# Kernel optimization log

Hardware: AMD Instinct MI355X
Metric: run time of the kernel (lower is better)

The kernel has to match this reference:

```python
import jax, jax.numpy as jnp
import numpy as np

N_HEADS = 8


def setup_inputs() -> dict:
    key = jax.random.key(0)
    k1, k2 = jax.random.split(key)
    image_qkv = jax.random.normal(k1, (2, 1536, 4096), dtype=jnp.float32)
    st_qkv = jax.random.normal(k2, (2, 1536, 1024), dtype=jnp.float32)
    return {"image_qkv": image_qkv, "st_qkv": st_qkv}


def reference(image_qkv, st_qkv):
    bs, width, img_len = image_qkv.shape
    st_len = st_qkv.shape[2]
    assert width % (3 * N_HEADS) == 0
    ch = width // (3 * N_HEADS)
    hc = N_HEADS * ch

    img_q, img_k, img_v = (image_qkv[:, i * hc:(i + 1) * hc] for i in range(3))
    st_q, st_k, st_v = (st_qkv[:, i * hc:(i + 1) * hc] for i in range(3))

    scale = 1.0 / jnp.sqrt(jnp.sqrt(jnp.float32(ch)))

    def split_heads(x, length):  # [bs, H*ch, L] -> [bs*H, ch, L]
        return x.reshape(bs * N_HEADS, ch, length)

    # image queries attend over st keys/values (softmax applied)
    w_i = jnp.einsum('bct,bcs->bts', split_heads(img_q, img_len) * scale,
                     split_heads(st_k, st_len) * scale)
    w_i = jax.nn.softmax(w_i.astype(jnp.float32), axis=-1).astype(w_i.dtype)
    attn_i = jnp.einsum('bts,bcs->bct', w_i, split_heads(st_v, st_len)).reshape(bs, -1, img_len)

    # st queries attend over image keys/values (NOTE: original code has NO softmax here)
    w_st = jnp.einsum('bct,bcs->bts', split_heads(st_q, st_len) * scale,
                      split_heads(img_k, img_len) * scale)
    attn_st = jnp.einsum('bts,bcs->bct', w_st, split_heads(img_v, img_len)).reshape(bs, -1, st_len)

    return attn_i, attn_st
```

## Files before the change

kernel.cpp:

```cpp
#include <hip/hip_runtime.h>
#include <hip/hip_bf16.h>
#include <stdint.h>

#define DEVI __device__ __forceinline__

typedef __attribute__((ext_vector_type(8))) short short8;
typedef __attribute__((ext_vector_type(16))) float f32x16;
typedef __attribute__((ext_vector_type(4))) float f32x4;
typedef __attribute__((ext_vector_type(2))) unsigned int uint2v;
typedef unsigned short ushortT;

union U8 { short8 s8; unsigned u[4]; };

DEVI unsigned short f2bf(float f) {
  unsigned u = __builtin_bit_cast(unsigned, f);
  u += 0x7fffu + ((u >> 16) & 1u);
  return (unsigned short)(u >> 16);
}
DEVI unsigned pk2(float lo, float hi) {
  return (unsigned)f2bf(lo) | ((unsigned)f2bf(hi) << 16);
}
DEVI unsigned cvtpk(float lo, float hi) {
  unsigned r;
  asm("v_cvt_pk_bf16_f32 %0, %1, %2" : "=v"(r) : "v"(lo), "v"(hi));
  return r;
}
DEVI float exp2a(float x) { return __builtin_amdgcn_exp2f(x); }

#define MFMA32 __builtin_amdgcn_mfma_f32_32x32x16_bf16
#define C_L2E 0.18033688011112042f

__global__ __launch_bounds__(256) void aux_kernel(
    const float* __restrict__ img, const float* __restrict__ st,
    ushortT* __restrict__ kfp, ushortT* __restrict__ vfp,
    float* __restrict__ Mws) {
  __shared__ __align__(16) char pool[32768];
  const int tid = threadIdx.x;
  const int bid = blockIdx.x;
  const int w = tid >> 6, lane = tid & 63, hi = lane >> 5, ln = lane & 31;

  if (bid < 256) {
    const int bh = bid >> 4, t = bid & 15;
    const int b = bh >> 3, h = bh & 7;
    const float* kbase = st + ((size_t)(b * 1536 + 512 + h * 64)) * 1024;
    const float* vbase = st + ((size_t)(b * 1536 + 1024 + h * 64)) * 1024;
    ushortT* ko = kfp + ((size_t)bh * 16 + t) * 4096;
    ushortT* vo = vfp + ((size_t)bh * 16 + t) * 4096;

    float (*kf)[65] = (float (*)[65])pool;
    {
      const int c = tid >> 2, s16 = (tid & 3) * 16;
      const float* kp = kbase + (size_t)c * 1024 + t * 64 + s16;
      f32x4 a = *(const f32x4*)kp, b4 = *(const f32x4*)(kp + 4),
            c4 = *(const f32x4*)(kp + 8), d4 = *(const f32x4*)(kp + 12);
#pragma unroll
      for (int j = 0; j < 4; ++j) {
        kf[c][s16 + j] = a[j];
        kf[c][s16 + 4 + j] = b4[j];
        kf[c][s16 + 8 + j] = c4[j];
        kf[c][s16 + 12 + j] = d4[j];
      }
    }
#pragma unroll
    for (int rep = 0; rep < 2; ++rep) {
      const int pair = tid + rep * 256;
      const int c = pair >> 3, oct = pair & 7;
      const float* vp = vbase + (size_t)c * 1024 + t * 64 + oct * 8;
      f32x4 lo = *(const f32x4*)vp, hp = *(const f32x4*)(vp + 4);
      uint2v la, ha;
      la[0] = pk2(lo[0], lo[1]); la[1] = pk2(lo[2], lo[3]);
      ha[0] = pk2(hp[0], hp[1]); ha[1] = pk2(hp[2], hp[3]);
      const int ci = c >> 5, lnn = c & 31;
      const int ss = oct >> 2, kk2 = (oct >> 1) & 1, o1 = oct & 1;
      const int f = ss * 4 + kk2 * 2 + ci;
      *(uint2v*)(vo + ((size_t)f * 64 + lnn) * 8 + o1 * 4) = la;
      *(uint2v*)(vo + ((size_t)f * 64 + 32 + lnn) * 8 + o1 * 4) = ha;
    }
    __syncthreads();
    {
      const int kk = w;
#pragma unroll
      for (int half = 0; half < 2; ++half) {
        float v8[8];
#pragma unroll
        for (int j = 0; j < 8; ++j) v8[j] = kf[kk * 16 + hi * 8 + j][half * 32 + ln];
        U8 u;
#pragma unroll
        for (int i = 0; i < 4; ++i) u.u[i] = pk2(v8[2 * i], v8[2 * i + 1]);
        *(short8*)(ko + ((size_t)(half * 4 + kk) * 64 + lane) * 8) = u.s8;
      }
    }
  } else {
    const int gb = bid - 256;
    const int bh = gb >> 3, chunk = gb & 7;
    const int b = bh >> 3, h = bh & 7;
    const float* kbase = img + ((size_t)(b * 1536 + 512 + h * 64)) * 4096;
    const float* vbase = img + ((size_t)(b * 1536 + 1024 + h * 64)) * 4096;

    f32x16 m00 = {}, m01 = {}, m10 = {}, m11 = {};
    const int sbeg = chunk * 512 + w * 128;
    for (int s0 = sbeg; s0 < sbeg + 128; s0 += 16) {
      const int sa = s0 + hi * 8;
      short8 av[2], bk[2];
#pragma unroll
      for (int ci = 0; ci < 2; ++ci) {
        const float* vp = vbase + (size_t)(ci * 32 + ln) * 4096 + sa;
        f32x4 lo = *(const f32x4*)vp, hp = *(const f32x4*)(vp + 4);
        U8 u;
        u.u[0] = pk2(lo[0], lo[1]); u.u[1] = pk2(lo[2], lo[3]);
        u.u[2] = pk2(hp[0], hp[1]); u.u[3] = pk2(hp[2], hp[3]);
        av[ci] = u.s8;
      }
#pragma unroll
      for (int cj = 0; cj < 2; ++cj) {
        const float* kp = kbase + (size_t)(cj * 32 + ln) * 4096 + sa;
        f32x4 lo = *(const f32x4*)kp, hp = *(const f32x4*)(kp + 4);
        U8 u;
        u.u[0] = pk2(lo[0], lo[1]); u.u[1] = pk2(lo[2], lo[3]);
        u.u[2] = pk2(hp[0], hp[1]); u.u[3] = pk2(hp[2], hp[3]);
        bk[cj] = u.s8;
      }
      m00 = MFMA32(av[0], bk[0], m00, 0, 0, 0);
      m01 = MFMA32(av[0], bk[1], m01, 0, 0, 0);
      m10 = MFMA32(av[1], bk[0], m10, 0, 0, 0);
      m11 = MFMA32(av[1], bk[1], m11, 0, 0, 0);
    }

    float (*part)[64][64] = (float (*)[64][64])pool;
    if (w < 2) {
#pragma unroll
      for (int q = 0; q < 16; ++q) {
        const int cr = (q & 3) + 8 * (q >> 2) + 4 * hi;
        part[w][cr][ln] = m00[q];
        part[w][cr][32 + ln] = m01[q];
        part[w][32 + cr][ln] = m10[q];
        part[w][32 + cr][32 + ln] = m11[q];
      }
    }
    __syncthreads();
    if (w >= 2) {
      const int pw = w - 2;
#pragma unroll
      for (int q = 0; q < 16; ++q) {
        const int cr = (q & 3) + 8 * (q >> 2) + 4 * hi;
        part[pw][cr][ln] += m00[q];
        part[pw][cr][32 + ln] += m01[q];
        part[pw][32 + cr][ln] += m10[q];
        part[pw][32 + cr][32 + ln] += m11[q];
      }
    }
    __syncthreads();
#pragma unroll
    for (int i = 0; i < 16; ++i) {
      const int e = tid + i * 256;
      const int c = e >> 6, cp = e & 63;
      Mws[(size_t)gb * 4096 + c * 64 + cp] =
          (part[0][c][cp] + part[1][c][cp]) * 0.125f;
    }
  }
}

DEVI void stage_tile(ushortT (*lds)[16][512], int buf, const ushortT* kf_all,
                     const ushortT* vf_all, int fpbase, int lane, int tile) {
#pragma unroll
  for (int j = 0; j < 4; ++j) {
    const int fp = fpbase + j;
    const ushortT* src =
        (fp < 8 ? kf_all + (size_t)tile * 4096 + (size_t)fp * 512
                : vf_all + (size_t)tile * 4096 + (size_t)(fp - 8) * 512) +
        lane * 8;
    __builtin_amdgcn_global_load_lds(
        (const __attribute__((address_space(1))) void*)src,
        (__attribute__((address_space(3))) void*)&lds[buf][fp][0], 16, 0, 0);
  }
}

DEVI void st2_body(const float* __restrict__ st, const float* __restrict__ Mws,
                   float* __restrict__ out1, int sb, int tid, char* pool) {
  const int bh = sb >> 2, tt = sb & 3;
  const int b = bh >> 3, h = bh & 7;
  const float* qbase = st + ((size_t)(b * 1536 + h * 64)) * 1024;
  float* o1 = out1 + ((size_t)(b * 512 + h * 64)) * 1024;
  char* msb = pool;

#pragma unroll
  for (int i = 0; i < 16; ++i) {
    const int e = tid + i * 256;
    const int c = e >> 6, cp = e & 63;
    const float* mp = Mws + (size_t)bh * 8 * 4096 + c * 64 + cp;
    float s = 0.f;
#pragma unroll
    for (int ch = 0; ch < 8; ++ch) s += mp[(size_t)ch * 4096];
    *(float*)(msb + c * 256 + ((cp * 4) ^ ((c & 7) << 5))) = s;
  }
  __syncthreads();

  const int w = tid >> 6, lane = tid & 63, hi = lane >> 5, ln = lane & 31;

  short8 aM0[4], aM1[4];
#pragma unroll
  for (int k = 0; k < 4; ++k) {
#pragma unroll
    for (int ci = 0; ci < 2; ++ci) {
      const int row = ci * 32 + ln;
      const int bo = k * 64 + hi * 32;
      const char* rp = msb + row * 256;
      const int swz = (row & 7) << 5;
      f32x4 lo = *(const f32x4*)(rp + (bo ^ swz));
      f32x4 hp = *(const f32x4*)(rp + ((bo + 16) ^ swz));
      U8 u;
      u.u[0] = pk2(lo[0], lo[1]); u.u[1] = pk2(lo[2], lo[3]);
      u.u[2] = pk2(hp[0], hp[1]); u.u[3] = pk2(hp[2], hp[3]);
      if (ci) aM1[k] = u.s8; else aM0[k] = u.s8;
    }
  }

#pragma unroll
  for (int nt = 0; nt < 2; ++nt) {
    const int t = tt * 256 + w * 64 + nt * 32 + ln;
    short8 bq[4];
#pragma unroll
    for (int k = 0; k < 4; ++k) {
      const float* qp = qbase + (size_t)(k * 16 + hi * 8) * 1024 + t;
      float q8[8];
#pragma unroll
      for (int j = 0; j < 8; ++j) q8[j] = qp[(size_t)j * 1024];
      U8 u;
#pragma unroll
      for (int i = 0; i < 4; ++i) u.u[i] = pk2(q8[2 * i], q8[2 * i + 1]);
      bq[k] = u.s8;
    }
    f32x16 a0 = {}, a1 = {};
#pragma unroll
    for (int k = 0; k < 4; ++k) {
      a0 = MFMA32(aM0[k], bq[k], a0, 0, 0, 0);
      a1 = MFMA32(aM1[k], bq[k], a1, 0, 0, 0);
    }
#pragma unroll
    for (int q = 0; q < 16; ++q) {
      const int cr = (q & 3) + 8 * (q >> 2) + 4 * hi;
      o1[(size_t)cr * 1024 + t] = a0[q];
      o1[(size_t)(cr + 32) * 1024 + t] = a1[q];
    }
  }
}

template <bool WITH_ST2>
__global__ __launch_bounds__(256, 3) void main_kernel(
    const float* __restrict__ img, const ushortT* __restrict__ kfp,
    const ushortT* __restrict__ vfp, const float* __restrict__ st,
    const float* __restrict__ Mws, float* __restrict__ out0,
    float* __restrict__ out1) {
  __shared__ __align__(16) char pool[32768];
  const int tid = threadIdx.x;
  const int bid = blockIdx.x;

  if (WITH_ST2 && bid >= 512) {
    st2_body(st, Mws, out1, bid - 512, tid, pool);
    return;
  }

  const int w = tid >> 6, lane = tid & 63, hi = lane >> 5, ln = lane & 31;
  const int bh = bid >> 5, tb = bid & 31;
  const int b = bh >> 3, h = bh & 7;
  const float* qbase = img + ((size_t)(b * 1536 + h * 64)) * 4096;
  float* obase = out0 + ((size_t)(b * 512 + h * 64)) * 4096;

  const int fpbase = w * 4;
  const int tcol = tb * 128 + w * 32 + ln;

  ushortT (*lds)[16][512] = (ushortT (*)[16][512])pool;
  const ushortT* kf_all = kfp + (size_t)bh * 16 * 4096;
  const ushortT* vf_all = vfp + (size_t)bh * 16 * 4096;

  stage_tile(lds, 0, kf_all, vf_all, fpbase, lane, 0);

  short8 qf[4];
#pragma unroll
  for (int k = 0; k < 4; ++k) {
    const float* qp = qbase + (size_t)(k * 16 + hi * 8) * 4096 + tcol;
    float q8[8];
#pragma unroll
    for (int j = 0; j < 8; ++j) q8[j] = qp[(size_t)j * 4096] * C_L2E;
    U8 u;
#pragma unroll
    for (int i = 0; i < 4; ++i) u.u[i] = pk2(q8[2 * i], q8[2 * i + 1]);
    qf[k] = u.s8;
  }

  f32x16 o0 = {}, o1 = {};
  float la0 = 0.f, la1 = 0.f, la2 = 0.f, la3 = 0.f;

  __syncthreads();

  for (int i = 0; i < 16; ++i) {
    const int cur = i & 1;
    const ushortT(*L)[512] = lds[cur];

    f32x16 sc0 = {}, sc1 = {};
    {
      short8 kfr[8];
#pragma unroll
      for (int f = 0; f < 8; ++f) kfr[f] = *(const short8*)&L[f][lane * 8];
      __builtin_amdgcn_s_setprio(1);
      sc0 = MFMA32(kfr[0], qf[0], sc0, 0, 0, 0);
      sc1 = MFMA32(kfr[4], qf[0], sc1, 0, 0, 0);
      sc0 = MFMA32(kfr[1], qf[1], sc0, 0, 0, 0);
      sc1 = MFMA32(kfr[5], qf[1], sc1, 0, 0, 0);
      sc0 = MFMA32(kfr[2], qf[2], sc0, 0, 0, 0);
      sc1 = MFMA32(kfr[6], qf[2], sc1, 0, 0, 0);
      sc0 = MFMA32(kfr[3], qf[3], sc0, 0, 0, 0);
      sc1 = MFMA32(kfr[7], qf[3], sc1, 0, 0, 0);
      __builtin_amdgcn_s_setprio(0);
    }

    if (i + 1 < 16)
      stage_tile(lds, cur ^ 1, kf_all, vf_all, fpbase, lane, i + 1);

#pragma unroll
    for (int q = 0; q < 16; q += 4) {
      float p0 = exp2a(sc0[q]);
      float p1 = exp2a(sc0[q + 1]);
      float p2 = exp2a(sc0[q + 2]);
      float p3 = exp2a(sc0[q + 3]);
      sc0[q] = p0; sc0[q + 1] = p1; sc0[q + 2] = p2; sc0[q + 3] = p3;
      la0 += p0; la1 += p1; la2 += p2; la3 += p3;
    }
#pragma unroll
    for (int q = 0; q < 16; q += 4) {
      float p0 = exp2a(sc1[q]);
      float p1 = exp2a(sc1[q + 1]);
      float p2 = exp2a(sc1[q + 2]);
      float p3 = exp2a(sc1[q + 3]);
      sc1[q] = p0; sc1[q + 1] = p1; sc1[q + 2] = p2; sc1[q + 3] = p3;
      la0 += p0; la1 += p1; la2 += p2; la3 += p3;
    }

#pragma unroll
    for (int ss = 0; ss < 2; ++ss) {
      const f32x16& sc = ss ? sc1 : sc0;
      U8 B0, B1;
      B0.u[0] = cvtpk(sc[0], sc[1]);   B0.u[1] = cvtpk(sc[2], sc[3]);
      B0.u[2] = cvtpk(sc[4], sc[5]);   B0.u[3] = cvtpk(sc[6], sc[7]);
      B1.u[0] = cvtpk(sc[8], sc[9]);   B1.u[1] = cvtpk(sc[10], sc[11]);
      B1.u[2] = cvtpk(sc[12], sc[13]); B1.u[3] = cvtpk(sc[14], sc[15]);
      short8 v00 = *(const short8*)&L[8 + ss * 4 + 0][lane * 8];
      short8 v01 = *(const short8*)&L[8 + ss * 4 + 1][lane * 8];
      short8 v10 = *(const short8*)&L[8 + ss * 4 + 2][lane * 8];
      short8 v11 = *(const short8*)&L[8 + ss * 4 + 3][lane * 8];
      __builtin_amdgcn_s_setprio(1);
      o0 = MFMA32(v00, B0.s8, o0, 0, 0, 0);
      o1 = MFMA32(v01, B0.s8, o1, 0, 0, 0);
      o0 = MFMA32(v10, B1.s8, o0, 0, 0, 0);
      o1 = MFMA32(v11, B1.s8, o1, 0, 0, 0);
      __builtin_amdgcn_s_setprio(0);
    }
    if (i + 1 < 16) __syncthreads();
  }

  float l = (la0 + la1) + (la2 + la3);
  l += __shfl_xor(l, 32);
  const float linv = 1.0f / l;
#pragma unroll
  for (int q = 0; q < 16; ++q) {
    const int c = (q & 3) + 8 * (q >> 2) + 4 * hi;
    obase[(size_t)c * 4096 + tcol] = o0[q] * linv;
    obase[(size_t)(c + 32) * 4096 + tcol] = o1[q] * linv;
  }
}

__global__ __launch_bounds__(256) void st2_kernel(
    const float* __restrict__ st, const float* __restrict__ Mws,
    float* __restrict__ out1) {
  __shared__ __align__(16) char pool[16384];
  st2_body(st, Mws, out1, blockIdx.x, threadIdx.x, pool);
}

extern "C" void kernel_launch(void* const* d_in, const int* in_sizes, int n_in,
                              void* d_out, int out_size, void* d_ws, size_t ws_size,
                              hipStream_t stream) {
  const float* img = (const float*)d_in[0];
  const float* st = (const float*)d_in[1];
  float* out0 = (float*)d_out;
  float* out1 = out0 + (size_t)2 * 512 * 4096;
  char* ws = (char*)d_ws;
  const size_t MB = 1u << 20;

  ushortT* kfp;
  ushortT* vfp;
  float* Ms;
  bool fits = ws_size >= 6 * MB;
  if (fits) {
    kfp = (ushortT*)ws; vfp = (ushortT*)(ws + 2 * MB); Ms = (float*)(ws + 4 * MB);
  } else {
    kfp = (ushortT*)out1; vfp = (ushortT*)((char*)out1 + 2 * MB);
    Ms = (float*)ws;
  }

  hipLaunchKernelGGL(aux_kernel, dim3(384), dim3(256), 0, stream, img, st, kfp,
                     vfp, Ms);
  if (fits) {
    hipLaunchKernelGGL((main_kernel<true>), dim3(576), dim3(256), 0, stream, img,
                       kfp, vfp, st, Ms, out0, out1);
  } else {
    hipLaunchKernelGGL((main_kernel<false>), dim3(512), dim3(256), 0, stream, img,
                       kfp, vfp, st, Ms, out0, out1);
    hipLaunchKernelGGL(st2_kernel, dim3(64), dim3(256), 0, stream, st, Ms, out1);
  }
}
```

Before: 44.06 us.

## Switch attention main kernel to 16x16x32 MFMA with 64-query tiles and interleaved KV

```diff
diff --git a/kernel.cpp b/kernel.cpp
--- a/kernel.cpp
+++ b/kernel.cpp
@@ -7,7 +7,6 @@
 typedef __attribute__((ext_vector_type(8))) short short8;
 typedef __attribute__((ext_vector_type(16))) float f32x16;
 typedef __attribute__((ext_vector_type(4))) float f32x4;
-typedef __attribute__((ext_vector_type(2))) unsigned int uint2v;
 typedef unsigned short ushortT;
 
 union U8 { short8 s8; unsigned u[4]; };
@@ -28,12 +27,12 @@
 DEVI float exp2a(float x) { return __builtin_amdgcn_exp2f(x); }
 
 #define MFMA32 __builtin_amdgcn_mfma_f32_32x32x16_bf16
+#define MFMA16 __builtin_amdgcn_mfma_f32_16x16x32_bf16
 #define C_L2E 0.18033688011112042f
 
 __global__ __launch_bounds__(256) void aux_kernel(
     const float* __restrict__ img, const float* __restrict__ st,
-    ushortT* __restrict__ kfp, ushortT* __restrict__ vfp,
-    float* __restrict__ Mws) {
+    ushortT* __restrict__ kvp, float* __restrict__ Mws) {
   __shared__ __align__(16) char pool[32768];
   const int tid = threadIdx.x;
   const int bid = blockIdx.x;
@@ -44,51 +43,52 @@
     const int b = bh >> 3, h = bh & 7;
     const float* kbase = st + ((size_t)(b * 1536 + 512 + h * 64)) * 1024;
     const float* vbase = st + ((size_t)(b * 1536 + 1024 + h * 64)) * 1024;
-    ushortT* ko = kfp + ((size_t)bh * 16 + t) * 4096;
-    ushortT* vo = vfp + ((size_t)bh * 16 + t) * 4096;
-
-    float (*kf)[65] = (float (*)[65])pool;
+    ushortT* tileo = kvp + ((size_t)bh * 16 + t) * 8192;
+
+    float (*kf)[68] = (float (*)[68])pool;
+
     {
       const int c = tid >> 2, s16 = (tid & 3) * 16;
       const float* kp = kbase + (size_t)c * 1024 + t * 64 + s16;
-      f32x4 a = *(const f32x4*)kp, b4 = *(const f32x4*)(kp + 4),
-            c4 = *(const f32x4*)(kp + 8), d4 = *(const f32x4*)(kp + 12);
-#pragma unroll
-      for (int j = 0; j < 4; ++j) {
-        kf[c][s16 + j] = a[j];
-        kf[c][s16 + 4 + j] = b4[j];
-        kf[c][s16 + 8 + j] = c4[j];
-        kf[c][s16 + 12 + j] = d4[j];
-      }
-    }
+#pragma unroll
+      for (int v = 0; v < 4; ++v)
+        *(f32x4*)&kf[c][s16 + v * 4] = *(const f32x4*)(kp + v * 4);
+    }
+    __syncthreads();
 #pragma unroll
     for (int rep = 0; rep < 2; ++rep) {
-      const int pair = tid + rep * 256;
-      const int c = pair >> 3, oct = pair & 7;
-      const float* vp = vbase + (size_t)c * 1024 + t * 64 + oct * 8;
-      f32x4 lo = *(const f32x4*)vp, hp = *(const f32x4*)(vp + 4);
-      uint2v la, ha;
-      la[0] = pk2(lo[0], lo[1]); la[1] = pk2(lo[2], lo[3]);
-      ha[0] = pk2(hp[0], hp[1]); ha[1] = pk2(hp[2], hp[3]);
-      const int ci = c >> 5, lnn = c & 31;
-      const int ss = oct >> 2, kk2 = (oct >> 1) & 1, o1 = oct & 1;
-      const int f = ss * 4 + kk2 * 2 + ci;
-      *(uint2v*)(vo + ((size_t)f * 64 + lnn) * 8 + o1 * 4) = la;
-      *(uint2v*)(vo + ((size_t)f * 64 + 32 + lnn) * 8 + o1 * 4) = ha;
-    }
-    __syncthreads();
-    {
-      const int kk = w;
-#pragma unroll
-      for (int half = 0; half < 2; ++half) {
-        float v8[8];
-#pragma unroll
-        for (int j = 0; j < 8; ++j) v8[j] = kf[kk * 16 + hi * 8 + j][half * 32 + ln];
-        U8 u;
-#pragma unroll
-        for (int i = 0; i < 4; ++i) u.u[i] = pk2(v8[2 * i], v8[2 * i + 1]);
-        *(short8*)(ko + ((size_t)(half * 4 + kk) * 64 + lane) * 8) = u.s8;
-      }
+      const int slot = tid + rep * 256;
+      const int frag = slot >> 6, l = slot & 63;
+      const int stile = frag >> 1, ks = frag & 1, g = l >> 4, r = l & 15;
+      float v8[8];
+#pragma unroll
+      for (int j = 0; j < 8; ++j) v8[j] = kf[ks * 32 + g * 8 + j][stile * 16 + r];
+      U8 u;
+#pragma unroll
+      for (int i = 0; i < 4; ++i) u.u[i] = pk2(v8[2 * i], v8[2 * i + 1]);
+      *(short8*)(tileo + ((size_t)frag * 64 + l) * 8) = u.s8;
+    }
+    __syncthreads();
+    {
+      const int c = tid >> 2, s16 = (tid & 3) * 16;
+      const float* vp = vbase + (size_t)c * 1024 + t * 64 + s16;
+#pragma unroll
+      for (int v = 0; v < 4; ++v)
+        *(f32x4*)&kf[c][s16 + v * 4] = *(const f32x4*)(vp + v * 4);
+    }
+    __syncthreads();
+#pragma unroll
+    for (int rep = 0; rep < 2; ++rep) {
+      const int slot = tid + rep * 256;
+      const int frag = slot >> 6, l = slot & 63;
+      const int ks2 = frag >> 2, ct = frag & 3, g = l >> 4, r = l & 15;
+      const int c = ct * 16 + r, s0 = ks2 * 32 + g * 4;
+      f32x4 lo = *(const f32x4*)&kf[c][s0];
+      f32x4 hp = *(const f32x4*)&kf[c][s0 + 16];
+      U8 u;
+      u.u[0] = pk2(lo[0], lo[1]); u.u[1] = pk2(lo[2], lo[3]);
+      u.u[2] = pk2(hp[0], hp[1]); u.u[3] = pk2(hp[2], hp[3]);
+      *(short8*)(tileo + ((size_t)(8 + frag) * 64 + l) * 8) = u.s8;
     }
   } else {
     const int gb = bid - 256;
@@ -160,15 +160,12 @@
   }
 }
 
-DEVI void stage_tile(ushortT (*lds)[16][512], int buf, const ushortT* kf_all,
-                     const ushortT* vf_all, int fpbase, int lane, int tile) {
+DEVI void stage_tile(ushortT (*lds)[16][512], int buf, const ushortT* kv_all,
+                     int fpbase, int lane, int tile) {
 #pragma unroll
   for (int j = 0; j < 4; ++j) {
     const int fp = fpbase + j;
-    const ushortT* src =
-        (fp < 8 ? kf_all + (size_t)tile * 4096 + (size_t)fp * 512
-                : vf_all + (size_t)tile * 4096 + (size_t)(fp - 8) * 512) +
-        lane * 8;
+    const ushortT* src = kv_all + (size_t)tile * 8192 + (size_t)fp * 512 + lane * 8;
     __builtin_amdgcn_global_load_lds(
         (const __attribute__((address_space(1))) void*)src,
         (__attribute__((address_space(3))) void*)&lds[buf][fp][0], 16, 0, 0);
@@ -247,125 +244,116 @@
 
 template <bool WITH_ST2>
 __global__ __launch_bounds__(256, 3) void main_kernel(
-    const float* __restrict__ img, const ushortT* __restrict__ kfp,
-    const ushortT* __restrict__ vfp, const float* __restrict__ st,
-    const float* __restrict__ Mws, float* __restrict__ out0,
-    float* __restrict__ out1) {
+    const float* __restrict__ img, const ushortT* __restrict__ kvp,
+    const float* __restrict__ st, const float* __restrict__ Mws,
+    float* __restrict__ out0, float* __restrict__ out1) {
   __shared__ __align__(16) char pool[32768];
   const int tid = threadIdx.x;
   const int bid = blockIdx.x;
 
-  if (WITH_ST2 && bid >= 512) {
-    st2_body(st, Mws, out1, bid - 512, tid, pool);
+  if (WITH_ST2 && bid >= 1024) {
+    st2_body(st, Mws, out1, bid - 1024, tid, pool);
     return;
   }
 
-  const int w = tid >> 6, lane = tid & 63, hi = lane >> 5, ln = lane & 31;
-  const int bh = bid >> 5, tb = bid & 31;
+  const int w = tid >> 6, lane = tid & 63, g = lane >> 4, r = lane & 15;
+  const int bh = bid >> 6, tb = bid & 63;
   const int b = bh >> 3, h = bh & 7;
   const float* qbase = img + ((size_t)(b * 1536 + h * 64)) * 4096;
   float* obase = out0 + ((size_t)(b * 512 + h * 64)) * 4096;
 
   const int fpbase = w * 4;
-  const int tcol = tb * 128 + w * 32 + ln;
+  const int tcol = tb * 64 + w * 16 + r;
 
   ushortT (*lds)[16][512] = (ushortT (*)[16][512])pool;
-  const ushortT* kf_all = kfp + (size_t)bh * 16 * 4096;
-  const ushortT* vf_all = vfp + (size_t)bh * 16 * 4096;
-
-  stage_tile(lds, 0, kf_all, vf_all, fpbase, lane, 0);
-
-  short8 qf[4];
-#pragma unroll
-  for (int k = 0; k < 4; ++k) {
-    const float* qp = qbase + (size_t)(k * 16 + hi * 8) * 4096 + tcol;
+  const ushortT* kv_all = kvp + (size_t)bh * 16 * 8192;
+
+  stage_tile(lds, 0, kv_all, fpbase, lane, 0);
+
+  short8 qf[2];
+#pragma unroll
+  for (int ks = 0; ks < 2; ++ks) {
+    const float* qp = qbase + (size_t)(ks * 32 + g * 8) * 4096 + tcol;
     float q8[8];
 #pragma unroll
     for (int j = 0; j < 8; ++j) q8[j] = qp[(size_t)j * 4096] * C_L2E;
     U8 u;
 #pragma unroll
     for (int i = 0; i < 4; ++i) u.u[i] = pk2(q8[2 * i], q8[2 * i + 1]);
-    qf[k] = u.s8;
-  }
-
-  f32x16 o0 = {}, o1 = {};
-  float la0 = 0.f, la1 = 0.f, la2 = 0.f, la3 = 0.f;
+    qf[ks] = u.s8;
+  }
+
+  f32x4 o0 = {}, o1 = {}, o2 = {}, o3 = {};
+  f32x4 la = {};
 
   __syncthreads();
 
   for (int i = 0; i < 16; ++i) {
-    const int cur = i & 1;
-    const ushortT(*L)[512] = lds[cur];
-
-    f32x16 sc0 = {}, sc1 = {};
+    const ushortT(*L)[512] = lds[i & 1];
+
+    f32x4 s0 = {}, s1 = {}, s2 = {}, s3 = {};
     {
       short8 kfr[8];
 #pragma unroll
       for (int f = 0; f < 8; ++f) kfr[f] = *(const short8*)&L[f][lane * 8];
       __builtin_amdgcn_s_setprio(1);
-      sc0 = MFMA32(kfr[0], qf[0], sc0, 0, 0, 0);
-      sc1 = MFMA32(kfr[4], qf[0], sc1, 0, 0, 0);
-      sc0 = MFMA32(kfr[1], qf[1], sc0, 0, 0, 0);
-      sc1 = MFMA32(kfr[5], qf[1], sc1, 0, 0, 0);
-      sc0 = MFMA32(kfr[2], qf[2], sc0, 0, 0, 0);
-      sc1 = MFMA32(kfr[6], qf[2], sc1, 0, 0, 0);
-      sc0 = MFMA32(kfr[3], qf[3], sc0, 0, 0, 0);
-      sc1 = MFMA32(kfr[7], qf[3], sc1, 0, 0, 0);
+      s0 = MFMA16(kfr[0], qf[0], s0, 0, 0, 0);
+      s1 = MFMA16(kfr[2], qf[0], s1, 0, 0, 0);
+      s2 = MFMA16(kfr[4], qf[0], s2, 0, 0, 0);
+      s3 = MFMA16(kfr[6], qf[0], s3, 0, 0, 0);
+      s0 = MFMA16(kfr[1], qf[1], s0, 0, 0, 0);
+      s1 = MFMA16(kfr[3], qf[1], s1, 0, 0, 0);
+      s2 = MFMA16(kfr[5], qf[1], s2, 0, 0, 0);
+      s3 = MFMA16(kfr[7], qf[1], s3, 0, 0, 0);
       __builtin_amdgcn_s_setprio(0);
     }
 
-    if (i + 1 < 16)
-      stage_tile(lds, cur ^ 1, kf_all, vf_all, fpbase, lane, i + 1);
-
-#pragma unroll
-    for (int q = 0; q < 16; q += 4) {
-      float p0 = exp2a(sc0[q]);
-      float p1 = exp2a(sc0[q + 1]);
-      float p2 = exp2a(sc0[q + 2]);
-      float p3 = exp2a(sc0[q + 3]);
-      sc0[q] = p0; sc0[q + 1] = p1; sc0[q + 2] = p2; sc0[q + 3] = p3;
-      la0 += p0; la1 += p1; la2 += p2; la3 += p3;
-    }
-#pragma unroll
-    for (int q = 0; q < 16; q += 4) {
-      float p0 = exp2a(sc1[q]);
-      float p1 = exp2a(sc1[q + 1]);
-      float p2 = exp2a(sc1[q + 2]);
-      float p3 = exp2a(sc1[q + 3]);
-      sc1[q] = p0; sc1[q + 1] = p1; sc1[q + 2] = p2; sc1[q + 3] = p3;
-      la0 += p0; la1 += p1; la2 += p2; la3 += p3;
-    }
-
-#pragma unroll
-    for (int ss = 0; ss < 2; ++ss) {
-      const f32x16& sc = ss ? sc1 : sc0;
-      U8 B0, B1;
-      B0.u[0] = cvtpk(sc[0], sc[1]);   B0.u[1] = cvtpk(sc[2], sc[3]);
-      B0.u[2] = cvtpk(sc[4], sc[5]);   B0.u[3] = cvtpk(sc[6], sc[7]);
-      B1.u[0] = cvtpk(sc[8], sc[9]);   B1.u[1] = cvtpk(sc[10], sc[11]);
-      B1.u[2] = cvtpk(sc[12], sc[13]); B1.u[3] = cvtpk(sc[14], sc[15]);
-      short8 v00 = *(const short8*)&L[8 + ss * 4 + 0][lane * 8];
-      short8 v01 = *(const short8*)&L[8 + ss * 4 + 1][lane * 8];
-      short8 v10 = *(const short8*)&L[8 + ss * 4 + 2][lane * 8];
-      short8 v11 = *(const short8*)&L[8 + ss * 4 + 3][lane * 8];
+    if (i + 1 < 16) stage_tile(lds, (i + 1) & 1, kv_all, fpbase, lane, i + 1);
+
+#pragma unroll
+    for (int q = 0; q < 4; ++q) { float p = exp2a(s0[q]); s0[q] = p; la[q] += p; }
+#pragma unroll
+    for (int q = 0; q < 4; ++q) { float p = exp2a(s1[q]); s1[q] = p; la[q] += p; }
+#pragma unroll
+    for (int q = 0; q < 4; ++q) { float p = exp2a(s2[q]); s2[q] = p; la[q] += p; }
+#pragma unroll
+    for (int q = 0; q < 4; ++q) { float p = exp2a(s3[q]); s3[q] = p; la[q] += p; }
+
+    {
+      U8 B;
+      B.u[0] = cvtpk(s0[0], s0[1]); B.u[1] = cvtpk(s0[2], s0[3]);
+      B.u[2] = cvtpk(s1[0], s1[1]); B.u[3] = cvtpk(s1[2], s1[3]);
       __builtin_amdgcn_s_setprio(1);
-      o0 = MFMA32(v00, B0.s8, o0, 0, 0, 0);
-      o1 = MFMA32(v01, B0.s8, o1, 0, 0, 0);
-      o0 = MFMA32(v10, B1.s8, o0, 0, 0, 0);
-      o1 = MFMA32(v11, B1.s8, o1, 0, 0, 0);
+      o0 = MFMA16(*(const short8*)&L[8][lane * 8], B.s8, o0, 0, 0, 0);
+      o1 = MFMA16(*(const short8*)&L[9][lane * 8], B.s8, o1, 0, 0, 0);
+      o2 = MFMA16(*(const short8*)&L[10][lane * 8], B.s8, o2, 0, 0, 0);
+      o3 = MFMA16(*(const short8*)&L[11][lane * 8], B.s8, o3, 0, 0, 0);
       __builtin_amdgcn_s_setprio(0);
     }
+    {
+      U8 B;
+      B.u[0] = cvtpk(s2[0], s2[1]); B.u[1] = cvtpk(s2[2], s2[3]);
+      B.u[2] = cvtpk(s3[0], s3[1]); B.u[3] = cvtpk(s3[2], s3[3]);
+      __builtin_amdgcn_s_setprio(1);
+      o0 = MFMA16(*(const short8*)&L[12][lane * 8], B.s8, o0, 0, 0, 0);
+      o1 = MFMA16(*(const short8*)&L[13][lane * 8], B.s8, o1, 0, 0, 0);
+      o2 = MFMA16(*(const short8*)&L[14][lane * 8], B.s8, o2, 0, 0, 0);
+      o3 = MFMA16(*(const short8*)&L[15][lane * 8], B.s8, o3, 0, 0, 0);
+      __builtin_amdgcn_s_setprio(0);
+    }
     if (i + 1 < 16) __syncthreads();
   }
 
-  float l = (la0 + la1) + (la2 + la3);
+  float l = (la[0] + la[1]) + (la[2] + la[3]);
+  l += __shfl_xor(l, 16);
   l += __shfl_xor(l, 32);
   const float linv = 1.0f / l;
 #pragma unroll
-  for (int q = 0; q < 16; ++q) {
-    const int c = (q & 3) + 8 * (q >> 2) + 4 * hi;
-    obase[(size_t)c * 4096 + tcol] = o0[q] * linv;
-    obase[(size_t)(c + 32) * 4096 + tcol] = o1[q] * linv;
+  for (int q = 0; q < 4; ++q) {
+    obase[(size_t)(g * 4 + q) * 4096 + tcol] = o0[q] * linv;
+    obase[(size_t)(16 + g * 4 + q) * 4096 + tcol] = o1[q] * linv;
+    obase[(size_t)(32 + g * 4 + q) * 4096 + tcol] = o2[q] * linv;
+    obase[(size_t)(48 + g * 4 + q) * 4096 + tcol] = o3[q] * linv;
   }
 }
 
@@ -386,25 +374,23 @@
   char* ws = (char*)d_ws;
   const size_t MB = 1u << 20;
 
-  ushortT* kfp;
-  ushortT* vfp;
+  ushortT* kvp;
   float* Ms;
   bool fits = ws_size >= 6 * MB;
   if (fits) {
-    kfp = (ushortT*)ws; vfp = (ushortT*)(ws + 2 * MB); Ms = (float*)(ws + 4 * MB);
+    kvp = (ushortT*)ws; Ms = (float*)(ws + 4 * MB);
   } else {
-    kfp = (ushortT*)out1; vfp = (ushortT*)((char*)out1 + 2 * MB);
+    kvp = (ushortT*)out1;
     Ms = (float*)ws;
   }
 
-  hipLaunchKernelGGL(aux_kernel, dim3(384), dim3(256), 0, stream, img, st, kfp,
-                     vfp, Ms);
+  hipLaunchKernelGGL(aux_kernel, dim3(384), dim3(256), 0, stream, img, st, kvp, Ms);
   if (fits) {
-    hipLaunchKernelGGL((main_kernel<true>), dim3(576), dim3(256), 0, stream, img,
-                       kfp, vfp, st, Ms, out0, out1);
+    hipLaunchKernelGGL((main_kernel<true>), dim3(1088), dim3(256), 0, stream, img,
+                       kvp, st, Ms, out0, out1);
   } else {
-    hipLaunchKernelGGL((main_kernel<false>), dim3(512), dim3(256), 0, stream, img,
-                       kfp, vfp, st, Ms, out0, out1);
+    hipLaunchKernelGGL((main_kernel<false>), dim3(1024), dim3(256), 0, stream, img,
+                       kvp, st, Ms, out0, out1);
     hipLaunchKernelGGL(st2_kernel, dim3(64), dim3(256), 0, stream, st, Ms, out1);
   }
 }
```

New measurement: 45.83 us. +4.0%, slower.
